# Performance work log

Hardware: AMD Instinct MI355X
Metric: run time of the kernel (lower is better)

Reference implementation:

```python
import jax, jax.numpy as jnp
import numpy as np

B, T, H, I, E = 2, 2048, 1024, 2048, 8
TOP_K = 2
RMS_EPS = 1e-6
ROUTING_GAIN = 1.0
INIT_STD = 0.02


def setup_inputs() -> dict:
    key = jax.random.key(0)
    ks = jax.random.split(key, 6)
    x = jax.random.normal(ks[0], (B, T, H), dtype=jnp.float32)
    q_norm_w = jnp.ones((H,), dtype=jnp.float32)
    k_proto = jax.random.normal(ks[1], (E, H), dtype=jnp.float32) * INIT_STD
    v_proto = jnp.eye(E, dtype=jnp.float32)  # nn.init.eye_
    gate_projs = jax.random.normal(ks[2], (E, H, I), dtype=jnp.float32) * INIT_STD
    up_projs = jax.random.normal(ks[3], (E, H, I), dtype=jnp.float32) * INIT_STD
    down_projs = jax.random.normal(ks[4], (E, I, H), dtype=jnp.float32) * INIT_STD
    return {"x": x, "q_norm_w": q_norm_w, "k_proto": k_proto, "v_proto": v_proto,
            "gate_projs": gate_projs, "up_projs": up_projs, "down_projs": down_projs}


def _routing_weights(x, q_norm_w, k_proto, v_proto):
    # CAPRRouter: RMSNorm -> proto attention -> softmax -> value mix -> gain
    q = x * jax.lax.rsqrt(jnp.mean(x * x, axis=-1, keepdims=True) + RMS_EPS) * q_norm_w
    attn = jax.nn.softmax(jnp.einsum('bth,ph->btp', q, k_proto) / np.sqrt(H).astype(np.float32), axis=-1)
    logits = jnp.einsum('btp,pq->btq', attn, v_proto) * ROUTING_GAIN
    rw = jax.nn.softmax(logits, axis=-1)  # [B,T,E]
    if TOP_K < E:
        tw, ti = jax.lax.top_k(rw, TOP_K)                       # [B,T,k]
        onehot = jax.nn.one_hot(ti, E, dtype=rw.dtype)          # [B,T,k,E]
        rw = jnp.einsum('btk,btke->bte', tw, onehot)            # scatter top-k back
        rw = rw / (jnp.sum(rw, axis=-1, keepdims=True) + 1e-9)
    return rw


def reference(x, q_norm_w, k_proto, v_proto, gate_projs, up_projs, down_projs):
    rw = _routing_weights(x, q_norm_w, k_proto, v_proto)  # [B,T,E]
    # Math-equivalent reassociation of torch's ('btp,phi->bthi' then 'bth,bthi->bti'):
    # per-expert GEMM then routing-weighted reduction over experts.
    gate_out = jnp.einsum('btp,btpi->bti', rw, jnp.einsum('bth,phi->btpi', x, gate_projs))
    up_out = jnp.einsum('btp,btpi->bti', rw, jnp.einsum('bth,phi->btpi', x, up_projs))
    intermediate = jax.nn.silu(gate_out) * up_out  # [B,T,I]
    output = jnp.einsum('btp,btph->bth', rw, jnp.einsum('bti,pih->btph', intermediate, down_projs))
    return output, rw
```

## Files before the change

kernel.cpp:

```cpp
#include <hip/hip_runtime.h>
#include <hip/hip_bf16.h>

#define NTOK 4096
#define HDIM 1024
#define IDIM 2048
#define NEXP 8
#define RBLK 16

typedef __attribute__((ext_vector_type(8))) short short8;
typedef __attribute__((ext_vector_type(4))) short short4b;
typedef __attribute__((ext_vector_type(4))) float f32x4;
typedef unsigned short ushort_t;

__device__ inline ushort_t f2bf(float f) {
    union { float f; unsigned u; } v; v.f = f;
    unsigned r = v.u + 0x7FFFu + ((v.u >> 16) & 1u);
    return (ushort_t)(r >> 16);
}
__device__ inline float bf2f(ushort_t h) {
    union { unsigned u; float f; } v; v.u = ((unsigned)h) << 16;
    return v.f;
}

#define GPTR(p) ((const __attribute__((address_space(1))) void*)(p))
#define LPTR(p) ((__attribute__((address_space(3))) void*)(p))

__global__ __launch_bounds__(256) void routing_kernel(
    const float* __restrict__ x, const float* __restrict__ qw,
    const float* __restrict__ kp, const float* __restrict__ vp,
    float* __restrict__ rw_out, int* __restrict__ counts,
    int* __restrict__ list, float2* __restrict__ topw,
    ushort_t* __restrict__ xb)
{
    __shared__ float kp_s[NEXP * HDIM];
    __shared__ float vp_s[NEXP * NEXP];
    __shared__ int lcnt[NEXP];
    __shared__ int base_s[NEXP];
    __shared__ int tinfo[RBLK][4];

    int tid = threadIdx.x;
    int wid = tid >> 6, lane = tid & 63;

    if (tid < NEXP) lcnt[tid] = 0;
    if (tid < NEXP * NEXP) vp_s[tid] = vp[tid];
    #pragma unroll
    for (int i = 0; i < 8; i++)
        ((float4*)kp_s)[tid + 256 * i] = ((const float4*)kp)[tid + 256 * i];

    float4 qv[4];
    #pragma unroll
    for (int j = 0; j < 4; j++) qv[j] = ((const float4*)qw)[lane + 64 * j];
    __syncthreads();

    for (int it = 0; it < RBLK / 4; it++) {
        int tl = wid * (RBLK / 4) + it;
        int t = blockIdx.x * RBLK + tl;
        const float4* xr4 = (const float4*)(x + (size_t)t * HDIM);
        float4 xv[4];
        #pragma unroll
        for (int j = 0; j < 4; j++) xv[j] = xr4[lane + 64 * j];

        ushort_t* xrow = xb + (size_t)t * HDIM;
        #pragma unroll
        for (int j = 0; j < 4; j++) {
            short4b o;
            o[0] = f2bf(xv[j].x); o[1] = f2bf(xv[j].y);
            o[2] = f2bf(xv[j].z); o[3] = f2bf(xv[j].w);
            ((short4b*)xrow)[lane + 64 * j] = o;
        }

        float ss = 0.f;
        #pragma unroll
        for (int j = 0; j < 4; j++)
            ss += xv[j].x*xv[j].x + xv[j].y*xv[j].y + xv[j].z*xv[j].z + xv[j].w*xv[j].w;
        #pragma unroll
        for (int off = 32; off; off >>= 1) ss += __shfl_xor(ss, off);
        float rms = rsqrtf(ss * (1.0f / HDIM) + 1e-6f);

        float4 q[4];
        #pragma unroll
        for (int j = 0; j < 4; j++) {
            q[j].x = xv[j].x * rms * qv[j].x; q[j].y = xv[j].y * rms * qv[j].y;
            q[j].z = xv[j].z * rms * qv[j].z; q[j].w = xv[j].w * rms * qv[j].w;
        }

        float d[NEXP];
        #pragma unroll
        for (int p = 0; p < NEXP; p++) {
            float acc = 0.f;
            #pragma unroll
            for (int j = 0; j < 4; j++) {
                float4 kv = ((const float4*)kp_s)[p * 256 + lane + 64 * j];
                acc += q[j].x*kv.x + q[j].y*kv.y + q[j].z*kv.z + q[j].w*kv.w;
            }
            #pragma unroll
            for (int off = 32; off; off >>= 1) acc += __shfl_xor(acc, off);
            d[p] = acc * (1.0f / 32.0f);
        }

        float m = d[0];
        #pragma unroll
        for (int p = 1; p < NEXP; p++) m = fmaxf(m, d[p]);
        float a[NEXP]; float s = 0.f;
        #pragma unroll
        for (int p = 0; p < NEXP; p++) { a[p] = expf(d[p] - m); s += a[p]; }
        float inv = 1.0f / s;
        #pragma unroll
        for (int p = 0; p < NEXP; p++) a[p] *= inv;
        float lg[NEXP];
        #pragma unroll
        for (int qi = 0; qi < NEXP; qi++) {
            float acc = 0.f;
            #pragma unroll
            for (int p = 0; p < NEXP; p++) acc += a[p] * vp_s[p * NEXP + qi];
            lg[qi] = acc;
        }
        float m2 = lg[0];
        #pragma unroll
        for (int p = 1; p < NEXP; p++) m2 = fmaxf(m2, lg[p]);
        float r[NEXP]; float s2 = 0.f;
        #pragma unroll
        for (int p = 0; p < NEXP; p++) { r[p] = expf(lg[p] - m2); s2 += r[p]; }
        float inv2 = 1.0f / s2;
        #pragma unroll
        for (int p = 0; p < NEXP; p++) r[p] *= inv2;
        int e0 = -1, e1 = -1; float w0 = -1.f, w1 = -1.f;
        #pragma unroll
        for (int p = 0; p < NEXP; p++) {
            if (r[p] > w0) { w1 = w0; e1 = e0; w0 = r[p]; e0 = p; }
            else if (r[p] > w1) { w1 = r[p]; e1 = p; }
        }
        float invn = 1.0f / (w0 + w1 + 1e-9f);
        float w0n = w0 * invn, w1n = w1 * invn;

        if (lane == 0) {
            #pragma unroll
            for (int p = 0; p < NEXP; p++)
                rw_out[(size_t)t * NEXP + p] = (p == e0) ? w0n : ((p == e1) ? w1n : 0.f);
            topw[t] = make_float2(w0n, w1n);
            int p0 = atomicAdd(&lcnt[e0], 1);
            int p1 = atomicAdd(&lcnt[e1], 1);
            tinfo[tl][0] = e0; tinfo[tl][1] = p0;
            tinfo[tl][2] = e1; tinfo[tl][3] = p1;
        }
    }
    __syncthreads();
    if (tid < NEXP) base_s[tid] = atomicAdd(&counts[tid], lcnt[tid]);
    __syncthreads();
    if (tid < RBLK) {
        int t = blockIdx.x * RBLK + tid;
        int e0 = tinfo[tid][0], p0 = tinfo[tid][1];
        int e1 = tinfo[tid][2], p1 = tinfo[tid][3];
        list[e0 * NTOK + base_s[e0] + p0] = t * 2;
        list[e1 * NTOK + base_s[e1] + p1] = t * 2 + 1;
    }
}

__global__ __launch_bounds__(256) void conv_t(const float* __restrict__ in, ushort_t* __restrict__ out,
                                              int K, int N) {
    __shared__ ushort_t ts[64][72];
    int e = blockIdx.z;
    int xb = blockIdx.x, yb = blockIdx.y;
    const float* ip = in + (size_t)e * K * N + (size_t)(yb * 64) * N + xb * 64;
    int NB = N / 128, KB = K / 64;
    int nb = xb >> 1, rhalf = (xb & 1) * 64;
    ushort_t* op = out + ((size_t)((size_t)e * NB + nb) * KB + yb) * (128 * 64);

    int tid = threadIdx.x;
    int r0 = tid >> 4;
    int c4 = (tid & 15) * 4;
    #pragma unroll
    for (int i = 0; i < 4; i++) {
        int r = r0 + i * 16;
        float4 v = *(const float4*)(ip + (size_t)r * N + c4);
        ts[c4+0][r] = f2bf(v.x); ts[c4+1][r] = f2bf(v.y);
        ts[c4+2][r] = f2bf(v.z); ts[c4+3][r] = f2bf(v.w);
    }
    __syncthreads();
    int n = tid >> 2;
    int kq = (tid & 3) * 16;
    int sw = (n & 7) << 3;
    short8 w0 = *(const short8*)&ts[n][kq];
    short8 w1 = *(const short8*)&ts[n][kq + 8];
    ushort_t* dst = op + (size_t)(rhalf + n) * 64;
    *(short8*)(dst + (kq ^ sw))       = w0;
    *(short8*)(dst + ((kq + 8) ^ sw)) = w1;
}

template<int K, int FUSED, int OUTBF>
__global__ __launch_bounds__(256) void gemm_bf16(
    const ushort_t* __restrict__ A,
    const ushort_t* __restrict__ W0, const ushort_t* __restrict__ W1,
    const int* __restrict__ counts, const int* __restrict__ list,
    void* __restrict__ out0, void* __restrict__ out1, int odim)
{
    constexpr int KB = K / 64;
    int e = blockIdx.z;
    int M = counts[e];
    int row0 = blockIdx.y * 128;
    if (row0 >= M) return;
    int nbTiles = odim / 128;
    int colb = blockIdx.x;
    const ushort_t* W = (FUSED && colb >= nbTiles) ? W1 : W0;
    void* outp        = (FUSED && colb >= nbTiles) ? out1 : out0;
    int nb = (FUSED && colb >= nbTiles) ? colb - nbTiles : colb;
    int col0 = nb * 128;

    __shared__ ushort_t Abuf[128 * 64];
    __shared__ ushort_t Bbuf[128 * 64];
    __shared__ int rowsS[128];

    int tid = threadIdx.x;
    if (tid < 128) {
        int r = row0 + tid;
        rowsS[tid] = (r < M) ? list[e * NTOK + r] : -1;
    }
    __syncthreads();

    int wid = tid >> 6, lane = tid & 63;
    int wr = wid >> 1, wc = wid & 1;
    int la = lane & 15, lb = lane >> 4;

    int swu = ((((lane & 7) * 16) ^ ((lane >> 3) << 4)) >> 1);
    const ushort_t* aP[4];
    #pragma unroll
    for (int i = 0; i < 4; i++) {
        int r = (wid * 4 + i) * 8 + (lane >> 3);
        int ent = rowsS[r];
        int tok = (ent >= 0) ? (ent >> 1) : 0;
        aP[i] = A + (size_t)tok * K + swu;
    }
    const ushort_t* Wt = W + (size_t)((size_t)e * nbTiles + nb) * KB * (128 * 64);

    int swr = (la & 7) << 3;
    int aoff[4][2], boff[4][2];
    #pragma unroll
    for (int m = 0; m < 4; m++)
        #pragma unroll
        for (int ks = 0; ks < 2; ks++)
            aoff[m][ks] = (wr * 64 + m * 16 + la) * 64 + ((ks * 32 + lb * 8) ^ swr);
    #pragma unroll
    for (int n = 0; n < 4; n++)
        #pragma unroll
        for (int ks = 0; ks < 2; ks++)
            boff[n][ks] = (wc * 64 + n * 16 + la) * 64 + ((ks * 32 + lb * 8) ^ swr);

    f32x4 acc[4][4];
    #pragma unroll
    for (int m = 0; m < 4; m++)
        #pragma unroll
        for (int n = 0; n < 4; n++) acc[m][n] = (f32x4){0.f, 0.f, 0.f, 0.f};

    for (int kt = 0; kt < KB; kt++) {
        #pragma unroll
        for (int i = 0; i < 4; i++) {
            int seg = wid * 4 + i;
            __builtin_amdgcn_global_load_lds(GPTR(aP[i] + kt * 64),
                                             LPTR(Abuf + seg * 512), 16, 0, 0);
            __builtin_amdgcn_global_load_lds(GPTR(Wt + (size_t)kt * 8192 + seg * 512 + lane * 8),
                                             LPTR(Bbuf + seg * 512), 16, 0, 0);
        }
        __syncthreads();
        #pragma unroll
        for (int ks = 0; ks < 2; ks++) {
            short8 af[4], bf[4];
            #pragma unroll
            for (int m = 0; m < 4; m++) af[m] = *(const short8*)&Abuf[aoff[m][ks]];
            #pragma unroll
            for (int n = 0; n < 4; n++) bf[n] = *(const short8*)&Bbuf[boff[n][ks]];
            #pragma unroll
            for (int m = 0; m < 4; m++)
                #pragma unroll
                for (int n = 0; n < 4; n++)
                    acc[m][n] = __builtin_amdgcn_mfma_f32_16x16x32_bf16(af[m], bf[n], acc[m][n], 0, 0, 0);
        }
        __syncthreads();
    }

    #pragma unroll
    for (int m = 0; m < 4; m++) {
        #pragma unroll
        for (int j = 0; j < 4; j++) {
            int rl = wr * 64 + m * 16 + lb * 4 + j;
            int ent = rowsS[rl];
            if (ent >= 0) {
                size_t base = (size_t)ent * odim + col0 + wc * 64 + la;
                #pragma unroll
                for (int n = 0; n < 4; n++) {
                    if (OUTBF) ((ushort_t*)outp)[base + n * 16] = f2bf(acc[m][n][j]);
                    else       ((float*)outp)[base + n * 16] = acc[m][n][j];
                }
            }
        }
    }
}

__global__ __launch_bounds__(256) void silu_mix(
    const ushort_t* __restrict__ bg, const ushort_t* __restrict__ bu,
    const float2* __restrict__ topw, ushort_t* __restrict__ inter)
{
    int idx = blockIdx.x * 256 + threadIdx.x;
    int t = idx >> 8;
    int i8 = (idx & 255) * 8;
    float2 w = topw[t];
    short8 g0 = *(const short8*)(bg + (size_t)(2*t)   * IDIM + i8);
    short8 g1 = *(const short8*)(bg + (size_t)(2*t+1) * IDIM + i8);
    short8 u0 = *(const short8*)(bu + (size_t)(2*t)   * IDIM + i8);
    short8 u1 = *(const short8*)(bu + (size_t)(2*t+1) * IDIM + i8);
    short8 r;
    #pragma unroll
    for (int j = 0; j < 8; j++) {
        float g = w.x * bf2f((ushort_t)g0[j]) + w.y * bf2f((ushort_t)g1[j]);
        float u = w.x * bf2f((ushort_t)u0[j]) + w.y * bf2f((ushort_t)u1[j]);
        float s = g / (1.f + expf(-g)) * u;
        r[j] = f2bf(s);
    }
    *(short8*)(inter + (size_t)t * IDIM + i8) = r;
}

__global__ __launch_bounds__(256) void out_mix(
    const float* __restrict__ pout, const float2* __restrict__ topw,
    float* __restrict__ out)
{
    int idx = blockIdx.x * 256 + threadIdx.x;
    int t = idx >> 8;
    int h4 = (idx & 255) * 4;
    float2 w = topw[t];
    float4 a = *(const float4*)(pout + (size_t)(2*t)   * HDIM + h4);
    float4 b = *(const float4*)(pout + (size_t)(2*t+1) * HDIM + h4);
    float4 r;
    r.x = w.x*a.x + w.y*b.x;
    r.y = w.x*a.y + w.y*b.y;
    r.z = w.x*a.z + w.y*b.z;
    r.w = w.x*a.w + w.y*b.w;
    *(float4*)(out + (size_t)t * HDIM + h4) = r;
}

extern "C" void kernel_launch(void* const* d_in, const int* in_sizes, int n_in,
                              void* d_out, int out_size, void* d_ws, size_t ws_size,
                              hipStream_t stream) {
    const float* x    = (const float*)d_in[0];
    const float* qw   = (const float*)d_in[1];
    const float* kp   = (const float*)d_in[2];
    const float* vp   = (const float*)d_in[3];
    const float* gate = (const float*)d_in[4];
    const float* up   = (const float*)d_in[5];
    const float* down = (const float*)d_in[6];
    float* out = (float*)d_out;
    float* rw_out = out + (size_t)NTOK * HDIM;

    char* ws = (char*)d_ws;
    int*      counts = (int*)ws;
    float2*   topw   = (float2*)(ws + 1024);
    int*      list   = (int*)(ws + 64 * 1024);
    ushort_t* xb     = (ushort_t*)(ws + 256 * 1024);
    ushort_t* wtg    = xb + (size_t)NTOK * HDIM;
    ushort_t* wtu    = wtg + (size_t)NEXP * HDIM * IDIM;
    ushort_t* wtd    = wtu + (size_t)NEXP * HDIM * IDIM;
    ushort_t* bg     = wtd + (size_t)NEXP * HDIM * IDIM;
    ushort_t* bu     = bg  + (size_t)2 * NTOK * IDIM;
    ushort_t* interb = bu  + (size_t)2 * NTOK * IDIM;
    float*    pout   = (float*)bg;

    hipMemsetAsync(counts, 0, NEXP * sizeof(int), stream);

    routing_kernel<<<NTOK / RBLK, 256, 0, stream>>>(x, qw, kp, vp, rw_out, counts, list, topw, xb);

    conv_t<<<dim3(IDIM / 64, HDIM / 64, NEXP), 256, 0, stream>>>(gate, wtg, HDIM, IDIM);
    conv_t<<<dim3(IDIM / 64, HDIM / 64, NEXP), 256, 0, stream>>>(up,   wtu, HDIM, IDIM);
    conv_t<<<dim3(HDIM / 64, IDIM / 64, NEXP), 256, 0, stream>>>(down, wtd, IDIM, HDIM);

    dim3 ggu(2 * IDIM / 128, NTOK / 128, NEXP);
    gemm_bf16<HDIM, 1, 1><<<ggu, 256, 0, stream>>>(xb, wtg, wtu, counts, list, bg, bu, IDIM);

    silu_mix<<<NTOK * IDIM / 8 / 256, 256, 0, stream>>>(bg, bu, topw, interb);

    dim3 gd(HDIM / 128, NTOK / 128, NEXP);
    gemm_bf16<IDIM, 0, 0><<<gd, 256, 0, stream>>>(interb, wtd, (const ushort_t*)nullptr,
                                                  counts, list, pout, nullptr, HDIM);

    out_mix<<<NTOK * HDIM / 4 / 256, 256, 0, stream>>>(pout, topw, out);
}
```

Baseline: 255.9 us.

## Rewrite expert GEMMs with 256-wide tiles and double-buffered LDS prefetch

Replaces the 128x128, 4-wave expert GEMM with a templated 512-thread kernel. Tiles are 256x256 for gate/up and 128x256 for down. The weight repack now writes 256-column tiles. The main loop double-buffers the A and B tiles in LDS and issues the next k-step's async global-to-LDS loads before computing the current one, so memory latency overlaps MFMA work. MFMA groups are split into phases with barriers and s_setprio. The larger tiles cut weight and activation reloads, at the cost of much more LDS per block (about 128KB for the gate/up GEMM), lower occupancy and more padding waste on partial expert row tiles.

Measured after the change: 359.4 us. 1.4x slower.

```diff
diff --git a/kernel.cpp b/kernel.cpp
--- a/kernel.cpp
+++ b/kernel.cpp
@@ -162,9 +162,9 @@
     int e = blockIdx.z;
     int xb = blockIdx.x, yb = blockIdx.y;
     const float* ip = in + (size_t)e * K * N + (size_t)(yb * 64) * N + xb * 64;
-    int NB = N / 128, KB = K / 64;
-    int nb = xb >> 1, rhalf = (xb & 1) * 64;
-    ushort_t* op = out + ((size_t)((size_t)e * NB + nb) * KB + yb) * (128 * 64);
+    int NB = N / 256, KB = K / 64;
+    int nb = xb >> 2, rq = (xb & 3) * 64;
+    ushort_t* op = out + ((size_t)((size_t)e * NB + nb) * KB + yb) * 16384;
 
     int tid = threadIdx.x;
     int r0 = tid >> 4;
@@ -182,111 +182,138 @@
     int sw = (n & 7) << 3;
     short8 w0 = *(const short8*)&ts[n][kq];
     short8 w1 = *(const short8*)&ts[n][kq + 8];
-    ushort_t* dst = op + (size_t)(rhalf + n) * 64;
+    ushort_t* dst = op + (size_t)(rq + n) * 64;
     *(short8*)(dst + (kq ^ sw))       = w0;
     *(short8*)(dst + ((kq + 8) ^ sw)) = w1;
 }
 
-template<int K, int FUSED, int OUTBF>
-__global__ __launch_bounds__(256) void gemm_bf16(
+template<int K, int BM, int MF, int FUSED, int OUTBF>
+__global__ __launch_bounds__(512, 2) void gemm8p(
     const ushort_t* __restrict__ A,
     const ushort_t* __restrict__ W0, const ushort_t* __restrict__ W1,
     const int* __restrict__ counts, const int* __restrict__ list,
     void* __restrict__ out0, void* __restrict__ out1, int odim)
 {
     constexpr int KB = K / 64;
+    constexpr int AHALF = BM * 64;
     int e = blockIdx.z;
     int M = counts[e];
-    int row0 = blockIdx.y * 128;
+    int row0 = blockIdx.y * BM;
     if (row0 >= M) return;
-    int nbTiles = odim / 128;
+    int nbTiles = odim / 256;
     int colb = blockIdx.x;
     const ushort_t* W = (FUSED && colb >= nbTiles) ? W1 : W0;
     void* outp        = (FUSED && colb >= nbTiles) ? out1 : out0;
     int nb = (FUSED && colb >= nbTiles) ? colb - nbTiles : colb;
-    int col0 = nb * 128;
-
-    __shared__ ushort_t Abuf[128 * 64];
-    __shared__ ushort_t Bbuf[128 * 64];
-    __shared__ int rowsS[128];
+    int col0 = nb * 256;
+
+    __shared__ ushort_t Abuf[2 * BM * 64];
+    __shared__ ushort_t Bbuf[2 * 256 * 64];
+    __shared__ int rowsS[BM];
 
     int tid = threadIdx.x;
-    if (tid < 128) {
-        int r = row0 + tid;
-        rowsS[tid] = (r < M) ? list[e * NTOK + r] : -1;
+    for (int i = tid; i < BM; i += 512) {
+        int r = row0 + i;
+        rowsS[i] = (r < M) ? list[e * NTOK + r] : -1;
     }
     __syncthreads();
 
     int wid = tid >> 6, lane = tid & 63;
-    int wr = wid >> 1, wc = wid & 1;
+    int wr = wid >> 2, wc = wid & 3;
     int la = lane & 15, lb = lane >> 4;
 
-    int swu = ((((lane & 7) * 16) ^ ((lane >> 3) << 4)) >> 1);
-    const ushort_t* aP[4];
-    #pragma unroll
-    for (int i = 0; i < 4; i++) {
-        int r = (wid * 4 + i) * 8 + (lane >> 3);
+    const ushort_t* aP[BM / 64];
+    #pragma unroll
+    for (int i = 0; i < BM / 64; ++i) {
+        int slot = tid + 512 * i;
+        int r = slot >> 3, c = slot & 7;
         int ent = rowsS[r];
         int tok = (ent >= 0) ? (ent >> 1) : 0;
-        aP[i] = A + (size_t)tok * K + swu;
-    }
-    const ushort_t* Wt = W + (size_t)((size_t)e * nbTiles + nb) * KB * (128 * 64);
-
-    int swr = (la & 7) << 3;
-    int aoff[4][2], boff[4][2];
-    #pragma unroll
-    for (int m = 0; m < 4; m++)
-        #pragma unroll
-        for (int ks = 0; ks < 2; ks++)
-            aoff[m][ks] = (wr * 64 + m * 16 + la) * 64 + ((ks * 32 + lb * 8) ^ swr);
-    #pragma unroll
-    for (int n = 0; n < 4; n++)
-        #pragma unroll
-        for (int ks = 0; ks < 2; ks++)
-            boff[n][ks] = (wc * 64 + n * 16 + la) * 64 + ((ks * 32 + lb * 8) ^ swr);
-
-    f32x4 acc[4][4];
-    #pragma unroll
-    for (int m = 0; m < 4; m++)
-        #pragma unroll
-        for (int n = 0; n < 4; n++) acc[m][n] = (f32x4){0.f, 0.f, 0.f, 0.f};
-
-    for (int kt = 0; kt < KB; kt++) {
-        #pragma unroll
-        for (int i = 0; i < 4; i++) {
-            int seg = wid * 4 + i;
+        aP[i] = A + (size_t)tok * K + ((c ^ (r & 7)) * 8);
+    }
+    const ushort_t* Wt = W + (size_t)((size_t)e * nbTiles + nb) * ((size_t)KB * 16384);
+
+    int aoff[MF][2], boff[4][2];
+    #pragma unroll
+    for (int m = 0; m < MF; ++m)
+        #pragma unroll
+        for (int ks = 0; ks < 2; ++ks)
+            aoff[m][ks] = (wr * (MF * 16) + m * 16 + la) * 64 + ((ks * 32 + lb * 8) ^ ((la & 7) << 3));
+    #pragma unroll
+    for (int n = 0; n < 4; ++n)
+        #pragma unroll
+        for (int ks = 0; ks < 2; ++ks)
+            boff[n][ks] = (wc * 64 + n * 16 + la) * 64 + ((ks * 32 + lb * 8) ^ ((la & 7) << 3));
+
+    f32x4 acc[MF][4];
+    #pragma unroll
+    for (int m = 0; m < MF; ++m)
+        #pragma unroll
+        for (int n = 0; n < 4; ++n) acc[m][n] = (f32x4){0.f, 0.f, 0.f, 0.f};
+
+    auto STAGE = [&](int kt, int d) {
+        #pragma unroll
+        for (int i = 0; i < BM / 64; ++i)
             __builtin_amdgcn_global_load_lds(GPTR(aP[i] + kt * 64),
-                                             LPTR(Abuf + seg * 512), 16, 0, 0);
-            __builtin_amdgcn_global_load_lds(GPTR(Wt + (size_t)kt * 8192 + seg * 512 + lane * 8),
-                                             LPTR(Bbuf + seg * 512), 16, 0, 0);
-        }
-        __syncthreads();
-        #pragma unroll
-        for (int ks = 0; ks < 2; ks++) {
-            short8 af[4], bf[4];
-            #pragma unroll
-            for (int m = 0; m < 4; m++) af[m] = *(const short8*)&Abuf[aoff[m][ks]];
-            #pragma unroll
-            for (int n = 0; n < 4; n++) bf[n] = *(const short8*)&Bbuf[boff[n][ks]];
-            #pragma unroll
-            for (int m = 0; m < 4; m++)
+                LPTR(Abuf + d * AHALF + (wid * 64 + 512 * i) * 8), 16, 0, 0);
+        #pragma unroll
+        for (int i = 0; i < 4; ++i)
+            __builtin_amdgcn_global_load_lds(GPTR(Wt + (size_t)kt * 16384 + (tid + 512 * i) * 8),
+                LPTR(Bbuf + d * 16384 + (wid * 64 + 512 * i) * 8), 16, 0, 0);
+    };
+
+    STAGE(0, 0);
+    asm volatile("s_waitcnt vmcnt(0)" ::: "memory");
+    __builtin_amdgcn_s_barrier();
+
+    for (int kt = 0; kt < KB; ++kt) {
+        const int cur = kt & 1;
+        if (kt + 1 < KB) STAGE(kt + 1, cur ^ 1);
+        const ushort_t* Ab = Abuf + cur * AHALF;
+        const ushort_t* Bb = Bbuf + cur * 16384;
+        #pragma unroll
+        for (int ph = 0; ph < 4; ++ph) {
+            const int mh = ph >> 1, nh = ph & 1;
+            short8 af[MF / 2][2], bfg[2][2];
+            #pragma unroll
+            for (int mm = 0; mm < MF / 2; ++mm)
                 #pragma unroll
-                for (int n = 0; n < 4; n++)
-                    acc[m][n] = __builtin_amdgcn_mfma_f32_16x16x32_bf16(af[m], bf[n], acc[m][n], 0, 0, 0);
-        }
-        __syncthreads();
-    }
-
-    #pragma unroll
-    for (int m = 0; m < 4; m++) {
-        #pragma unroll
-        for (int j = 0; j < 4; j++) {
-            int rl = wr * 64 + m * 16 + lb * 4 + j;
+                for (int ks = 0; ks < 2; ++ks)
+                    af[mm][ks] = *(const short8*)&Ab[aoff[mh * (MF / 2) + mm][ks]];
+            #pragma unroll
+            for (int nn = 0; nn < 2; ++nn)
+                #pragma unroll
+                for (int ks = 0; ks < 2; ++ks)
+                    bfg[nn][ks] = *(const short8*)&Bb[boff[nh * 2 + nn][ks]];
+            __builtin_amdgcn_s_barrier();
+            __builtin_amdgcn_s_setprio(1);
+            #pragma unroll
+            for (int mm = 0; mm < MF / 2; ++mm)
+                #pragma unroll
+                for (int nn = 0; nn < 2; ++nn)
+                    #pragma unroll
+                    for (int ks = 0; ks < 2; ++ks)
+                        acc[mh * (MF / 2) + mm][nh * 2 + nn] =
+                            __builtin_amdgcn_mfma_f32_16x16x32_bf16(
+                                af[mm][ks], bfg[nn][ks],
+                                acc[mh * (MF / 2) + mm][nh * 2 + nn], 0, 0, 0);
+            __builtin_amdgcn_s_setprio(0);
+            __builtin_amdgcn_s_barrier();
+        }
+        asm volatile("s_waitcnt vmcnt(0)" ::: "memory");
+        __builtin_amdgcn_s_barrier();
+    }
+
+    #pragma unroll
+    for (int m = 0; m < MF; ++m) {
+        #pragma unroll
+        for (int j = 0; j < 4; ++j) {
+            int rl = wr * (MF * 16) + m * 16 + lb * 4 + j;
             int ent = rowsS[rl];
             if (ent >= 0) {
                 size_t base = (size_t)ent * odim + col0 + wc * 64 + la;
                 #pragma unroll
-                for (int n = 0; n < 4; n++) {
+                for (int n = 0; n < 4; ++n) {
                     if (OUTBF) ((ushort_t*)outp)[base + n * 16] = f2bf(acc[m][n][j]);
                     else       ((float*)outp)[base + n * 16] = acc[m][n][j];
                 }
@@ -370,14 +397,14 @@
     conv_t<<<dim3(IDIM / 64, HDIM / 64, NEXP), 256, 0, stream>>>(up,   wtu, HDIM, IDIM);
     conv_t<<<dim3(HDIM / 64, IDIM / 64, NEXP), 256, 0, stream>>>(down, wtd, IDIM, HDIM);
 
-    dim3 ggu(2 * IDIM / 128, NTOK / 128, NEXP);
-    gemm_bf16<HDIM, 1, 1><<<ggu, 256, 0, stream>>>(xb, wtg, wtu, counts, list, bg, bu, IDIM);
+    dim3 ggu(2 * IDIM / 256, NTOK / 256, NEXP);
+    gemm8p<HDIM, 256, 8, 1, 1><<<ggu, 512, 0, stream>>>(xb, wtg, wtu, counts, list, bg, bu, IDIM);
 
     silu_mix<<<NTOK * IDIM / 8 / 256, 256, 0, stream>>>(bg, bu, topw, interb);
 
-    dim3 gd(HDIM / 128, NTOK / 128, NEXP);
-    gemm_bf16<IDIM, 0, 0><<<gd, 256, 0, stream>>>(interb, wtd, (const ushort_t*)nullptr,
-                                                  counts, list, pout, nullptr, HDIM);
+    dim3 gd(HDIM / 256, NTOK / 128, NEXP);
+    gemm8p<IDIM, 128, 4, 0, 0><<<gd, 512, 0, stream>>>(interb, wtd, (const ushort_t*)nullptr,
+                                                       counts, list, pout, nullptr, HDIM);
 
     out_mix<<<NTOK * HDIM / 4 / 256, 256, 0, stream>>>(pout, topw, out);
 }
```

## Split down-projection GEMM along K into two partial sums reduced in out_mix

Applied to the files above, without the earlier changes.

The down-projection grouped GEMM now splits its K dimension (IDIM) into two halves, launching twice as many blocks, each writing an fp32 partial result into a separate buffer region. out_mix sums the two partials before applying the routing weights. This aims to raise parallelism and balance across CUs, at the cost of doubled partial-output writes and reads.

Result: slower. 267.1 us (+4.4%).

```diff
diff --git a/kernel.cpp b/kernel.cpp
--- a/kernel.cpp
+++ b/kernel.cpp
@@ -187,15 +187,20 @@
     *(short8*)(dst + ((kq + 8) ^ sw)) = w1;
 }
 
-template<int K, int FUSED, int OUTBF>
+template<int KLEN, int KTOT, int FUSED, int OUTBF, int SPLITK>
 __global__ __launch_bounds__(256) void gemm_bf16(
     const ushort_t* __restrict__ A,
     const ushort_t* __restrict__ W0, const ushort_t* __restrict__ W1,
     const int* __restrict__ counts, const int* __restrict__ list,
     void* __restrict__ out0, void* __restrict__ out1, int odim)
 {
-    constexpr int KB = K / 64;
-    int e = blockIdx.z;
+    constexpr int KB = KLEN / 64;
+    constexpr int KBTOT = KTOT / 64;
+    int zz = blockIdx.z;
+    int e      = SPLITK ? (zz & (NEXP - 1)) : zz;
+    int ksplit = SPLITK ? (zz >> 3) : 0;
+    int koff   = ksplit * KLEN;
+
     int M = counts[e];
     int row0 = blockIdx.y * 128;
     if (row0 >= M) return;
@@ -228,9 +233,10 @@
         int r = (wid * 4 + i) * 8 + (lane >> 3);
         int ent = rowsS[r];
         int tok = (ent >= 0) ? (ent >> 1) : 0;
-        aP[i] = A + (size_t)tok * K + swu;
-    }
-    const ushort_t* Wt = W + (size_t)((size_t)e * nbTiles + nb) * KB * (128 * 64);
+        aP[i] = A + (size_t)tok * KTOT + koff + swu;
+    }
+    const ushort_t* Wt = W + (size_t)((size_t)e * nbTiles + nb) * ((size_t)KBTOT * 8192)
+                           + (size_t)(koff / 64) * 8192;
 
     int swr = (la & 7) << 3;
     int aoff[4][2], boff[4][2];
@@ -287,8 +293,12 @@
                 size_t base = (size_t)ent * odim + col0 + wc * 64 + la;
                 #pragma unroll
                 for (int n = 0; n < 4; n++) {
-                    if (OUTBF) ((ushort_t*)outp)[base + n * 16] = f2bf(acc[m][n][j]);
-                    else       ((float*)outp)[base + n * 16] = acc[m][n][j];
+                    if (OUTBF) {
+                        ((ushort_t*)outp)[base + n * 16] = f2bf(acc[m][n][j]);
+                    } else {
+                        float* oF = (float*)outp + (size_t)ksplit * 2 * NTOK * odim;
+                        oF[base + n * 16] = acc[m][n][j];
+                    }
                 }
             }
         }
@@ -322,17 +332,20 @@
     const float* __restrict__ pout, const float2* __restrict__ topw,
     float* __restrict__ out)
 {
+    const size_t SPLITSZ = (size_t)2 * NTOK * HDIM;
     int idx = blockIdx.x * 256 + threadIdx.x;
     int t = idx >> 8;
     int h4 = (idx & 255) * 4;
     float2 w = topw[t];
-    float4 a = *(const float4*)(pout + (size_t)(2*t)   * HDIM + h4);
-    float4 b = *(const float4*)(pout + (size_t)(2*t+1) * HDIM + h4);
+    float4 a0 = *(const float4*)(pout + (size_t)(2*t)   * HDIM + h4);
+    float4 b0 = *(const float4*)(pout + (size_t)(2*t+1) * HDIM + h4);
+    float4 a1 = *(const float4*)(pout + SPLITSZ + (size_t)(2*t)   * HDIM + h4);
+    float4 b1 = *(const float4*)(pout + SPLITSZ + (size_t)(2*t+1) * HDIM + h4);
     float4 r;
-    r.x = w.x*a.x + w.y*b.x;
-    r.y = w.x*a.y + w.y*b.y;
-    r.z = w.x*a.z + w.y*b.z;
-    r.w = w.x*a.w + w.y*b.w;
+    r.x = w.x*(a0.x + a1.x) + w.y*(b0.x + b1.x);
+    r.y = w.x*(a0.y + a1.y) + w.y*(b0.y + b1.y);
+    r.z = w.x*(a0.z + a1.z) + w.y*(b0.z + b1.z);
+    r.w = w.x*(a0.w + a1.w) + w.y*(b0.w + b1.w);
     *(float4*)(out + (size_t)t * HDIM + h4) = r;
 }
 
@@ -371,13 +384,13 @@
     conv_t<<<dim3(HDIM / 64, IDIM / 64, NEXP), 256, 0, stream>>>(down, wtd, IDIM, HDIM);
 
     dim3 ggu(2 * IDIM / 128, NTOK / 128, NEXP);
-    gemm_bf16<HDIM, 1, 1><<<ggu, 256, 0, stream>>>(xb, wtg, wtu, counts, list, bg, bu, IDIM);
+    gemm_bf16<HDIM, HDIM, 1, 1, 0><<<ggu, 256, 0, stream>>>(xb, wtg, wtu, counts, list, bg, bu, IDIM);
 
     silu_mix<<<NTOK * IDIM / 8 / 256, 256, 0, stream>>>(bg, bu, topw, interb);
 
-    dim3 gd(HDIM / 128, NTOK / 128, NEXP);
-    gemm_bf16<IDIM, 0, 0><<<gd, 256, 0, stream>>>(interb, wtd, (const ushort_t*)nullptr,
-                                                  counts, list, pout, nullptr, HDIM);
+    dim3 gd(HDIM / 128, NTOK / 128, 2 * NEXP);
+    gemm_bf16<IDIM / 2, IDIM, 0, 0, 1><<<gd, 256, 0, stream>>>(interb, wtd, (const ushort_t*)nullptr,
+                                                               counts, list, pout, nullptr, HDIM);
 
     out_mix<<<NTOK * HDIM / 4 / 256, 256, 0, stream>>>(pout, topw, out);
 }
```

## Stage GEMM epilogue through LDS for vectorized bf16 stores, down-proj output in bf16

Applied to the files above, without the earlier changes.

The GEMM epilogue now writes the accumulator tile into padded shared memory and then issues coalesced 16-byte bf16 row stores to the scattered token rows, replacing the per-element strided writes. The down-projection partial output is switched from fp32 to bf16, which halves its write and read traffic, and out_mix is adjusted to read bf16 in 8-element chunks. This adds an extra bf16 rounding on the per-expert down output before the routing mix, and enlarges shared memory per block. The A-load swizzle expression is also rewritten.

Measured after the change: 251.5 us (median of 4 runs). Within noise of the previous version (-1.7%).

```diff
diff --git a/kernel.cpp b/kernel.cpp
--- a/kernel.cpp
+++ b/kernel.cpp
@@ -187,12 +187,12 @@
     *(short8*)(dst + ((kq + 8) ^ sw)) = w1;
 }
 
-template<int K, int FUSED, int OUTBF>
+template<int K, int FUSED>
 __global__ __launch_bounds__(256) void gemm_bf16(
     const ushort_t* __restrict__ A,
     const ushort_t* __restrict__ W0, const ushort_t* __restrict__ W1,
     const int* __restrict__ counts, const int* __restrict__ list,
-    void* __restrict__ out0, void* __restrict__ out1, int odim)
+    ushort_t* __restrict__ out0, ushort_t* __restrict__ out1, int odim)
 {
     constexpr int KB = K / 64;
     int e = blockIdx.z;
@@ -202,13 +202,14 @@
     int nbTiles = odim / 128;
     int colb = blockIdx.x;
     const ushort_t* W = (FUSED && colb >= nbTiles) ? W1 : W0;
-    void* outp        = (FUSED && colb >= nbTiles) ? out1 : out0;
+    ushort_t* outp    = (FUSED && colb >= nbTiles) ? out1 : out0;
     int nb = (FUSED && colb >= nbTiles) ? colb - nbTiles : colb;
     int col0 = nb * 128;
 
-    __shared__ ushort_t Abuf[128 * 64];
-    __shared__ ushort_t Bbuf[128 * 64];
+    __shared__ ushort_t smem[128 * 136];
     __shared__ int rowsS[128];
+    ushort_t* Abuf = smem;
+    ushort_t* Bbuf = smem + 8192;
 
     int tid = threadIdx.x;
     if (tid < 128) {
@@ -221,7 +222,7 @@
     int wr = wid >> 1, wc = wid & 1;
     int la = lane & 15, lb = lane >> 4;
 
-    int swu = ((((lane & 7) * 16) ^ ((lane >> 3) << 4)) >> 1);
+    int swu = (((lane & 7) ^ (lane >> 3)) * 8);
     const ushort_t* aP[4];
     #pragma unroll
     for (int i = 0; i < 4; i++) {
@@ -230,7 +231,7 @@
         int tok = (ent >= 0) ? (ent >> 1) : 0;
         aP[i] = A + (size_t)tok * K + swu;
     }
-    const ushort_t* Wt = W + (size_t)((size_t)e * nbTiles + nb) * KB * (128 * 64);
+    const ushort_t* Wt = W + (size_t)((size_t)e * nbTiles + nb) * ((size_t)KB * 8192);
 
     int swr = (la & 7) << 3;
     int aoff[4][2], boff[4][2];
@@ -277,21 +278,24 @@
         __syncthreads();
     }
 
-    #pragma unroll
-    for (int m = 0; m < 4; m++) {
-        #pragma unroll
-        for (int j = 0; j < 4; j++) {
-            int rl = wr * 64 + m * 16 + lb * 4 + j;
-            int ent = rowsS[rl];
-            if (ent >= 0) {
-                size_t base = (size_t)ent * odim + col0 + wc * 64 + la;
-                #pragma unroll
-                for (int n = 0; n < 4; n++) {
-                    if (OUTBF) ((ushort_t*)outp)[base + n * 16] = f2bf(acc[m][n][j]);
-                    else       ((float*)outp)[base + n * 16] = acc[m][n][j];
-                }
-            }
-        }
+    ushort_t* ob = smem;
+    #pragma unroll
+    for (int m = 0; m < 4; m++)
+        #pragma unroll
+        for (int n = 0; n < 4; n++)
+            #pragma unroll
+            for (int j = 0; j < 4; j++)
+                ob[(wr * 64 + m * 16 + lb * 4 + j) * 136 + wc * 64 + n * 16 + la] =
+                    f2bf(acc[m][n][j]);
+    __syncthreads();
+    int ch = tid & 15, rg = tid >> 4;
+    #pragma unroll
+    for (int i = 0; i < 8; i++) {
+        int r = i * 16 + rg;
+        int ent = rowsS[r];
+        short8 v = *(const short8*)&ob[r * 136 + ch * 8];
+        if (ent >= 0)
+            *(short8*)(outp + (size_t)ent * odim + col0 + ch * 8) = v;
     }
 }
 
@@ -319,21 +323,27 @@
 }
 
 __global__ __launch_bounds__(256) void out_mix(
-    const float* __restrict__ pout, const float2* __restrict__ topw,
+    const ushort_t* __restrict__ pout, const float2* __restrict__ topw,
     float* __restrict__ out)
 {
     int idx = blockIdx.x * 256 + threadIdx.x;
-    int t = idx >> 8;
-    int h4 = (idx & 255) * 4;
+    int t = idx >> 7;
+    int h8 = (idx & 127) * 8;
     float2 w = topw[t];
-    float4 a = *(const float4*)(pout + (size_t)(2*t)   * HDIM + h4);
-    float4 b = *(const float4*)(pout + (size_t)(2*t+1) * HDIM + h4);
-    float4 r;
-    r.x = w.x*a.x + w.y*b.x;
-    r.y = w.x*a.y + w.y*b.y;
-    r.z = w.x*a.z + w.y*b.z;
-    r.w = w.x*a.w + w.y*b.w;
-    *(float4*)(out + (size_t)t * HDIM + h4) = r;
+    short8 a = *(const short8*)(pout + (size_t)(2*t)   * HDIM + h8);
+    short8 b = *(const short8*)(pout + (size_t)(2*t+1) * HDIM + h8);
+    float4 r0, r1;
+    r0.x = w.x*bf2f((ushort_t)a[0]) + w.y*bf2f((ushort_t)b[0]);
+    r0.y = w.x*bf2f((ushort_t)a[1]) + w.y*bf2f((ushort_t)b[1]);
+    r0.z = w.x*bf2f((ushort_t)a[2]) + w.y*bf2f((ushort_t)b[2]);
+    r0.w = w.x*bf2f((ushort_t)a[3]) + w.y*bf2f((ushort_t)b[3]);
+    r1.x = w.x*bf2f((ushort_t)a[4]) + w.y*bf2f((ushort_t)b[4]);
+    r1.y = w.x*bf2f((ushort_t)a[5]) + w.y*bf2f((ushort_t)b[5]);
+    r1.z = w.x*bf2f((ushort_t)a[6]) + w.y*bf2f((ushort_t)b[6]);
+    r1.w = w.x*bf2f((ushort_t)a[7]) + w.y*bf2f((ushort_t)b[7]);
+    float* op = out + (size_t)t * HDIM + h8;
+    *(float4*)op       = r0;
+    *(float4*)(op + 4) = r1;
 }
 
 extern "C" void kernel_launch(void* const* d_in, const int* in_sizes, int n_in,
@@ -360,7 +370,7 @@
     ushort_t* bg     = wtd + (size_t)NEXP * HDIM * IDIM;
     ushort_t* bu     = bg  + (size_t)2 * NTOK * IDIM;
     ushort_t* interb = bu  + (size_t)2 * NTOK * IDIM;
-    float*    pout   = (float*)bg;
+    ushort_t* pout   = bg;
 
     hipMemsetAsync(counts, 0, NEXP * sizeof(int), stream);
 
@@ -371,13 +381,13 @@
     conv_t<<<dim3(HDIM / 64, IDIM / 64, NEXP), 256, 0, stream>>>(down, wtd, IDIM, HDIM);
 
     dim3 ggu(2 * IDIM / 128, NTOK / 128, NEXP);
-    gemm_bf16<HDIM, 1, 1><<<ggu, 256, 0, stream>>>(xb, wtg, wtu, counts, list, bg, bu, IDIM);
+    gemm_bf16<HDIM, 1><<<ggu, 256, 0, stream>>>(xb, wtg, wtu, counts, list, bg, bu, IDIM);
 
     silu_mix<<<NTOK * IDIM / 8 / 256, 256, 0, stream>>>(bg, bu, topw, interb);
 
     dim3 gd(HDIM / 128, NTOK / 128, NEXP);
-    gemm_bf16<IDIM, 0, 0><<<gd, 256, 0, stream>>>(interb, wtd, (const ushort_t*)nullptr,
-                                                  counts, list, pout, nullptr, HDIM);
-
-    out_mix<<<NTOK * HDIM / 4 / 256, 256, 0, stream>>>(pout, topw, out);
-}
+    gemm_bf16<IDIM, 0><<<gd, 256, 0, stream>>>(interb, wtd, (const ushort_t*)nullptr,
+                                               counts, list, pout, nullptr, HDIM);
+
+    out_mix<<<NTOK * HDIM / 8 / 256, 256, 0, stream>>>(pout, topw, out);
+}
```
